# Performance work log

Hardware: AMD Instinct MI355X
Metric: run time of the kernel (lower is better)

The kernel has to match this reference:

```python
import jax, jax.numpy as jnp
import numpy as np

Q_HEADS, KV_HEADS, DIMS, IN_DIMS = 16, 4, 1024, 1024
HEAD_D = DIMS // Q_HEADS            # 64
GROUPS = Q_HEADS // KV_HEADS        # 4
ROPE_BASE = 10000.0


def nd_rope(x, coords):
    """N-D rotary embedding.
    x: [..., s, d]; coords: broadcastable [..., s, a] (float).
    Head dim d is split into a contiguous chunks of d//a; within each chunk
    consecutive pairs (2i, 2i+1) are rotated by angle coord_axis * base^(-2i/(d//a)).
    """
    a = coords.shape[-1]
    d = x.shape[-1]
    dpa = d // a                                  # dims per coordinate axis (even)
    inv_freq = ROPE_BASE ** (-jnp.arange(dpa // 2, dtype=jnp.float32) * (2.0 / dpa))
    angles = coords[..., :, None] * inv_freq      # [..., s, a, dpa//2]
    angles = angles.reshape(angles.shape[:-2] + (d // 2,))
    cos, sin = jnp.cos(angles), jnp.sin(angles)
    xp = x.reshape(x.shape[:-1] + (d // 2, 2))
    x1, x2 = xp[..., 0], xp[..., 1]
    return jnp.stack([x1 * cos - x2 * sin, x1 * sin + x2 * cos], axis=-1).reshape(x.shape)


def setup_inputs() -> dict:
    key = jax.random.key(0)
    k1, k2, k3, k4, k5, k6, k7, k8 = jax.random.split(key, 8)
    B, SQ, SKV, A = 4, 2048, 2048, 2
    q = jax.random.normal(k1, (B, SQ, IN_DIMS), dtype=jnp.float32)
    kv = jax.random.normal(k2, (B, SKV, IN_DIMS), dtype=jnp.float32)
    q_coords = jax.random.randint(k3, (B, SQ, A), 0, 2048, dtype=jnp.int32)
    kv_coords = jax.random.randint(k4, (B, SKV, A), 0, 2048, dtype=jnp.int32)
    s_in = 1.0 / np.sqrt(IN_DIMS)
    Wq = jax.random.normal(k5, (IN_DIMS, Q_HEADS, HEAD_D), dtype=jnp.float32) * s_in
    Wk = jax.random.normal(k6, (IN_DIMS, KV_HEADS, HEAD_D), dtype=jnp.float32) * s_in
    Wv = jax.random.normal(k7, (IN_DIMS, KV_HEADS, HEAD_D), dtype=jnp.float32) * s_in
    Wo = jax.random.normal(k8, (KV_HEADS * HEAD_D, IN_DIMS), dtype=jnp.float32) * (1.0 / np.sqrt(KV_HEADS * HEAD_D))
    return {"q": q, "q_coords": q_coords, "kv": kv, "kv_coords": kv_coords,
            "Wq": Wq, "Wk": Wk, "Wv": Wv, "Wo": Wo}


def reference(q, q_coords, kv, kv_coords, Wq, Wk, Wv, Wo):
    B, SQ = q.shape[0], q.shape[1]
    qp = jnp.einsum('bsi,ihd->bshd', q, Wq)   # [b, sq, q_heads, hd]
    kp = jnp.einsum('bsi,ihd->bshd', kv, Wk)  # [b, skv, kv_heads, hd]
    vp = jnp.einsum('bsi,ihd->bshd', kv, Wv)
    # '... s (h g) d -> ... g h s d' with h=KV_HEADS outer, g=GROUPS inner
    qp = qp.reshape(B, SQ, KV_HEADS, GROUPS, HEAD_D).transpose(0, 3, 2, 1, 4)  # [b,g,h,sq,hd]
    kp = kp.transpose(0, 2, 1, 3)  # [b,h,skv,hd]
    vp = vp.transpose(0, 2, 1, 3)
    qc = q_coords.astype(jnp.float32)[:, None, None]  # [b,1,1,sq,a] -> broadcast over g,h
    kc = kv_coords.astype(jnp.float32)[:, None]       # [b,1,skv,a] -> broadcast over h
    qr = nd_rope(qp, qc)
    kr = nd_rope(kp, kc)
    # NOTE: einops pattern omits g in output -> group axis is SUMMED (faithful to source)
    scores = jnp.einsum('bghsd,bhad->bhsa', qr, kr) / (HEAD_D ** 0.5)
    attn = jax.nn.softmax(scores, axis=-1)
    out = jnp.einsum('bhsa,bhad->bhsd', attn, vp)
    out = out.transpose(0, 2, 1, 3).reshape(B, SQ, KV_HEADS * HEAD_D)
    return out @ Wo
```

## Files before the change

### kernel.cpp

```cpp
#include <hip/hip_runtime.h>

#define BATCH 4
#define SEQQ  2048
#define SEQKV 2048
#define NH    4
#define HD    64
#define IND   1024
#define QSCL 0.18033688011112042f

typedef __attribute__((ext_vector_type(8))) short short8;
typedef __attribute__((ext_vector_type(4))) short s4v;
typedef __attribute__((ext_vector_type(4))) float floatx4;

#if defined(__HIP_DEVICE_COMPILE__) && __has_builtin(__builtin_amdgcn_exp2f)
  #define EXP2(x) __builtin_amdgcn_exp2f(x)
#else
  #define EXP2(x) exp2f(x)
#endif

#if defined(__HIP_DEVICE_COMPILE__)
  #if __has_builtin(__builtin_amdgcn_mfma_f32_16x16x16bf16_1k)
    #define MFMA16(a, b, c) __builtin_amdgcn_mfma_f32_16x16x16bf16_1k(a, b, c, 0, 0, 0)
  #elif __has_builtin(__builtin_amdgcn_mfma_f32_16x16x16_bf16)
    #define MFMA16(a, b, c) __builtin_amdgcn_mfma_f32_16x16x16_bf16(a, b, c, 0, 0, 0)
  #else
    #error "no 16x16x16 bf16 MFMA builtin on gfx950 device pass"
  #endif
#else
  #define MFMA16(a, b, c) (c)
#endif
#define MFMA32(a, b, c) __builtin_amdgcn_mfma_f32_16x16x32_bf16(a, b, c, 0, 0, 0)

__device__ __forceinline__ short f2b(float f) {
    unsigned u; __builtin_memcpy(&u, &f, 4);
    u = (u + 0x7fffu + ((u >> 16) & 1u)) >> 16;
    return (short)u;
}
__device__ __forceinline__ short8 cvt8(const float* p) {
    float4 a = *(const float4*)p;
    float4 b = *(const float4*)(p + 4);
    short8 r;
    r[0] = f2b(a.x); r[1] = f2b(a.y); r[2] = f2b(a.z); r[3] = f2b(a.w);
    r[4] = f2b(b.x); r[5] = f2b(b.y); r[6] = f2b(b.z); r[7] = f2b(b.w);
    return r;
}

__global__ __launch_bounds__(256) void prep_all(
    const float* __restrict__ Wq, const float* __restrict__ Wk,
    const float* __restrict__ Wv, const float* __restrict__ Wo,
    const float* __restrict__ q, const float* __restrict__ kv,
    short* __restrict__ Wq_t, short* __restrict__ Wkv_t, short* __restrict__ Wo_t,
    short* __restrict__ qb, short* __restrict__ kvb) {
    __shared__ short Ts[64][65];
    int blk = blockIdx.x;
    if (blk < 256) {
        int c4 = threadIdx.x & 63, r4 = threadIdx.x >> 6;
        if (blk < 64) {
            int h = blk & 3, ib = blk >> 2;
#pragma unroll 4
            for (int jj = 0; jj < 16; ++jj) {
                int il = r4 * 16 + jj;
                float s = 0.f;
#pragma unroll
                for (int g = 0; g < 4; ++g)
                    s += Wq[(ib * 64 + il) * 1024 + (h * 4 + g) * 64 + c4];
                Ts[il][c4] = f2b(s);
            }
            __syncthreads();
#pragma unroll 4
            for (int jj = 0; jj < 16; ++jj) {
                int dl = r4 * 16 + jj;
                Wq_t[(h * 64 + dl) * 1024 + ib * 64 + c4] = Ts[c4][dl];
            }
        } else if (blk < 192) {
            int t = blk - 64, ss = t >> 6; t &= 63;
            int ib = t >> 2, nb = t & 3;
            const float* W = ss ? Wv : Wk;
#pragma unroll 4
            for (int jj = 0; jj < 16; ++jj) {
                int il = r4 * 16 + jj;
                Ts[il][c4] = f2b(W[(ib * 64 + il) * 256 + nb * 64 + c4]);
            }
            __syncthreads();
#pragma unroll 4
            for (int jj = 0; jj < 16; ++jj) {
                int dl = r4 * 16 + jj;
                Wkv_t[(ss * 256 + nb * 64 + dl) * 1024 + ib * 64 + c4] = Ts[c4][dl];
            }
        } else {
            int t = blk - 192, kb = t >> 4, nb = t & 15;
#pragma unroll 4
            for (int jj = 0; jj < 16; ++jj) {
                int il = r4 * 16 + jj;
                Ts[il][c4] = f2b(Wo[(kb * 64 + il) * 1024 + nb * 64 + c4]);
            }
            __syncthreads();
#pragma unroll 4
            for (int jj = 0; jj < 16; ++jj) {
                int dl = r4 * 16 + jj;
                Wo_t[(nb * 64 + dl) * 256 + kb * 64 + c4] = Ts[c4][dl];
            }
        }
    } else if (blk < 4352) {
        long e = ((long)(blk - 256) * 256 + threadIdx.x) * 8;
        *(short8*)(qb + e) = cvt8(q + e);
    } else {
        long e = ((long)(blk - 4352) * 256 + threadIdx.x) * 8;
        *(short8*)(kvb + e) = cvt8(kv + e);
    }
}

__device__ __forceinline__ void gemm128_body(
    const short* __restrict__ A, const short* __restrict__ Wt, float* __restrict__ C,
    int m0, int n0, int N, int K, short* As, short* Bs) {
    const int t = threadIdx.x;
    const int w = t >> 6, lane = t & 63, ln = lane & 15, quad = lane >> 4;
    const int wm = w >> 1, wn = w & 1;
    const int srow = lane >> 2, skc = (lane & 3) * 8;
    floatx4 acc[4][4];
#pragma unroll
    for (int mt = 0; mt < 4; ++mt)
#pragma unroll
        for (int nt = 0; nt < 4; ++nt) acc[mt][nt] = floatx4{0.f, 0.f, 0.f, 0.f};

    for (int ks = 0; ks < K; ks += 32) {
        __syncthreads();
#pragma unroll
        for (int i = 0; i < 2; ++i) {
            __builtin_amdgcn_global_load_lds(
                (const void*)(A + (long)(m0 + w * 32 + i * 16 + srow) * K + ks + skc),
                (void*)(As + (w * 2 + i) * 512), 16, 0, 0);
            __builtin_amdgcn_global_load_lds(
                (const void*)(Wt + (long)(n0 + w * 32 + i * 16 + srow) * K + ks + skc),
                (void*)(Bs + (w * 2 + i) * 512), 16, 0, 0);
        }
        __syncthreads();
        short8 af[4], bf[4];
#pragma unroll
        for (int mt = 0; mt < 4; ++mt)
            af[mt] = *(const short8*)(As + (wm * 64 + mt * 16 + ln) * 32 + quad * 8);
#pragma unroll
        for (int nt = 0; nt < 4; ++nt)
            bf[nt] = *(const short8*)(Bs + (wn * 64 + nt * 16 + ln) * 32 + quad * 8);
#pragma unroll
        for (int mt = 0; mt < 4; ++mt)
#pragma unroll
            for (int nt = 0; nt < 4; ++nt)
                acc[mt][nt] = MFMA32(af[mt], bf[nt], acc[mt][nt]);
    }
#pragma unroll
    for (int mt = 0; mt < 4; ++mt) {
        int row0 = m0 + wm * 64 + mt * 16 + quad * 4;
#pragma unroll
        for (int nt = 0; nt < 4; ++nt) {
            int col = n0 + wn * 64 + nt * 16 + ln;
#pragma unroll
            for (int r = 0; r < 4; ++r)
                C[(long)(row0 + r) * N + col] = acc[mt][nt][r];
        }
    }
}

__global__ __launch_bounds__(256) void proj_gemm(
    const short* __restrict__ qb, const short* __restrict__ kvb,
    const short* __restrict__ Wq_t, const short* __restrict__ Wkv_t,
    float* __restrict__ Qp, float* __restrict__ KVp) {
    __shared__ __align__(16) short As[128 * 32];
    __shared__ __align__(16) short Bs[128 * 32];
    int id = blockIdx.x;
    if (id < 128)
        gemm128_body(qb, Wq_t, Qp, (id >> 1) * 128, (id & 1) * 128, 256, 1024, As, Bs);
    else {
        int t = id - 128;
        gemm128_body(kvb, Wkv_t, KVp, (t >> 2) * 128, (t & 3) * 128, 512, 1024, As, Bs);
    }
}

__global__ __launch_bounds__(256) void final_gemm(
    const short* __restrict__ Ob, const short* __restrict__ Wo_t, float* __restrict__ out) {
    __shared__ __align__(16) short As[128 * 32];
    __shared__ __align__(16) short Bs[128 * 32];
    gemm128_body(Ob, Wo_t, out, blockIdx.x * 128, blockIdx.y * 128, 1024, 256, As, Bs);
}

__global__ __launch_bounds__(256) void rope_all(
    const float* __restrict__ Qp, const int* __restrict__ qc,
    const float* __restrict__ KVp, const int* __restrict__ kvc,
    short* __restrict__ Qr, short* __restrict__ Kr, short* __restrict__ Vt) {
    __shared__ __align__(16) short Ts[64][72];
    int blk = blockIdx.x;
    if (blk < 8192) {
        bool isq = blk < 4096;
        int idx = (isq ? blk : blk - 4096) * 256 + threadIdx.x;
        int j = idx & 31, h = (idx >> 5) & 3, s = (idx >> 7) & 2047, b = idx >> 18;
        int bs = b * 2048 + s;
        const float* src = isq ? (Qp + (long)bs * 256) : (KVp + (long)bs * 512);
        float2 x = *(const float2*)(src + h * 64 + 2 * j);
        float c = (float)(isq ? qc : kvc)[bs * 2 + (j >> 4)];
        float ang = c * __expf((float)(j & 15) * -0.5756462732485114f);
        float sn, cs; __sincosf(ang, &sn, &cs);
        if (isq) { sn *= QSCL; cs *= QSCL; }
        short2 o; o.x = f2b(x.x * cs - x.y * sn); o.y = f2b(x.x * sn + x.y * cs);
        short* dst = isq ? Qr : Kr;
        *(short2*)(dst + (long)((b * 4 + h) * 2048 + s) * 64 + 2 * j) = o;
    } else {
        int t2 = blk - 8192;
        int bh = t2 & 15, kt = (t2 >> 4) << 6;
        int b = bh >> 2, h = bh & 3;
        {
            int r = threadIdx.x >> 2, c = (threadIdx.x & 3) << 4;
            const float* src = KVp + (long)(b * 2048 + kt + r) * 512 + 256 + h * 64 + c;
#pragma unroll
            for (int j = 0; j < 16; ++j) Ts[c + j][r] = f2b(src[j]);
        }
        __syncthreads();
        {
            int d = threadIdx.x >> 2, c = (threadIdx.x & 3) << 4;
            long dst = ((long)bh * 64 + d) * 2048 + kt + c;
            *(short8*)(Vt + dst)     = *(const short8*)(&Ts[d][c]);
            *(short8*)(Vt + dst + 8) = *(const short8*)(&Ts[d][c + 8]);
        }
    }
}

__global__ __launch_bounds__(256, 4) void attn_kernel(
    const short* __restrict__ Qr, const short* __restrict__ Kr,
    const short* __restrict__ Vt, float* __restrict__ Op, float* __restrict__ Lp) {
    __shared__ __align__(16) short Kls[64 * 64];
    __shared__ __align__(16) short Vls[64 * 64];
    const int blk = blockIdx.x;
    const int bh = blk & 15, sp = (blk >> 4) & 3, qg = blk >> 6;
    const int w = threadIdx.x >> 6, lane = threadIdx.x & 63;
    const int ln = lane & 15, quad = lane >> 4;
    const int q0 = qg * 128 + w * 32;
    const short* Qb = Qr + (long)bh * SEQKV * HD;
    const short* Kb = Kr + (long)bh * SEQKV * HD;
    const short* Vb = Vt + (long)bh * HD * SEQKV;

    const int srow = lane >> 3;
    const int schk = (lane & 7) ^ (srow & 7);
    const long kstage0 = (long)(w * 16 + srow) * HD + schk * 8;
    const long vstage0 = (long)(w * 16 + srow) * SEQKV + schk * 8;

    short8 qf[2][2];
#pragma unroll
    for (int qs = 0; qs < 2; ++qs)
#pragma unroll
        for (int ck = 0; ck < 2; ++ck)
            qf[qs][ck] = *(const short8*)(Qb + (long)(q0 + qs * 16 + ln) * HD + ck * 32 + quad * 8);

    s4v ones;
#pragma unroll
    for (int j = 0; j < 4; ++j) ones[j] = (short)0x3F80;

    floatx4 o[2][4], ol[2];
#pragma unroll
    for (int qs = 0; qs < 2; ++qs) {
        ol[qs] = floatx4{0.f, 0.f, 0.f, 0.f};
#pragma unroll
        for (int nt = 0; nt < 4; ++nt) o[qs][nt] = floatx4{0.f, 0.f, 0.f, 0.f};
    }

    const int ln7 = ln & 7;
    int koff[2];
#pragma unroll
    for (int ck = 0; ck < 2; ++ck) koff[ck] = ln * 64 + ((ck * 4 + quad) ^ ln7) * 8;
    int voff[4];
#pragma unroll
    for (int t = 0; t < 4; ++t) voff[t] = ln * 64 + ((t * 2 + (quad >> 1)) ^ ln7) * 8 + (quad & 1) * 4;

    for (int kt = sp * 512; kt < sp * 512 + 512; kt += 64) {
        __syncthreads();
#pragma unroll
        for (int i = 0; i < 2; ++i) {
            __builtin_amdgcn_global_load_lds(
                (const void*)(Kb + (long)kt * HD + kstage0 + (long)i * 8 * HD),
                (void*)(Kls + (w * 16 + i * 8) * 64), 16, 0, 0);
            __builtin_amdgcn_global_load_lds(
                (const void*)(Vb + kt + vstage0 + (long)i * 8 * SEQKV),
                (void*)(Vls + (w * 16 + i * 8) * 64), 16, 0, 0);
        }
        __syncthreads();

#pragma unroll
        for (int t = 0; t < 4; ++t) {
            short8 a0 = *(const short8*)(Kls + t * 1024 + koff[0]);
            short8 a1 = *(const short8*)(Kls + t * 1024 + koff[1]);
            floatx4 st0 = {0.f, 0.f, 0.f, 0.f}, st1 = {0.f, 0.f, 0.f, 0.f};
            st0 = MFMA32(a0, qf[0][0], st0);
            st1 = MFMA32(a0, qf[1][0], st1);
            st0 = MFMA32(a1, qf[0][1], st0);
            st1 = MFMA32(a1, qf[1][1], st1);
            s4v pt0, pt1;
#pragma unroll
            for (int j = 0; j < 4; ++j) {
                float p0 = EXP2(st0[j]);
                float p1 = EXP2(st1[j]);
                unsigned u0, u1;
                __builtin_memcpy(&u0, &p0, 4); __builtin_memcpy(&u1, &p1, 4);
                pt0[j] = (short)((u0 + 0x8000u) >> 16);
                pt1[j] = (short)((u1 + 0x8000u) >> 16);
            }
#pragma unroll
            for (int nt = 0; nt < 4; ++nt) {
                s4v vf = *(const s4v*)(Vls + nt * 1024 + voff[t]);
                o[0][nt] = MFMA16(vf, pt0, o[0][nt]);
                o[1][nt] = MFMA16(vf, pt1, o[1][nt]);
            }
            ol[0] = MFMA16(ones, pt0, ol[0]);
            ol[1] = MFMA16(ones, pt1, ol[1]);
        }
    }
#pragma unroll
    for (int qs = 0; qs < 2; ++qs) {
        long qrow = (long)(sp * 16 + bh) * 2048 + q0 + qs * 16 + ln;
        if (quad == 0) Lp[qrow] = ol[qs][0];
#pragma unroll
        for (int nt = 0; nt < 4; ++nt)
            *(floatx4*)(Op + qrow * 64 + nt * 16 + quad * 4) = o[qs][nt];
    }
}

__global__ __launch_bounds__(256) void combine_kernel(
    const float* __restrict__ Op, const float* __restrict__ Lp, short* __restrict__ Ob) {
    int row = blockIdx.x * 4 + (threadIdx.x >> 6);
    int d = threadIdx.x & 63;
    int bh = row >> 11, qq = row & 2047;
    int b = bh >> 2, h = bh & 3;
    float os = 0.f, ls = 0.f;
#pragma unroll
    for (int s = 0; s < 4; ++s) {
        long rr = (long)(s * 16 + bh) * 2048 + qq;
        os += Op[rr * 64 + d];
        ls += Lp[rr];
    }
    Ob[((long)(b * 2048 + qq)) * 256 + h * 64 + d] = f2b(os / ls);
}

extern "C" void kernel_launch(void* const* d_in, const int* in_sizes, int n_in,
                              void* d_out, int out_size, void* d_ws, size_t ws_size,
                              hipStream_t stream) {
    const float* q   = (const float*)d_in[0];
    const int*   qc  = (const int*)d_in[1];
    const float* kv  = (const float*)d_in[2];
    const int*   kvc = (const int*)d_in[3];
    const float* Wq  = (const float*)d_in[4];
    const float* Wk  = (const float*)d_in[5];
    const float* Wv  = (const float*)d_in[6];
    const float* Wo  = (const float*)d_in[7];
    float* out = (float*)d_out;

    char* ws = (char*)d_ws;
    const size_t MB = 1024 * 1024;
    short* Wq_t  = (short*)(ws);
    short* Wkv_t = (short*)(ws + MB / 2);
    short* Wo_t  = (short*)(ws + 3 * MB / 2);
    short* qb    = (short*)(ws + 2 * MB);
    short* kvb   = (short*)(ws + 18 * MB);
    float* Qp    = (float*)(ws + 34 * MB);
    float* KVp   = (float*)(ws + 42 * MB);
    short* Qr    = (short*)(ws + 2 * MB);
    short* Kr    = (short*)(ws + 6 * MB);
    short* Vt    = (short*)(ws + 10 * MB);
    short* Ob    = (short*)(ws + 14 * MB);
    float* Opart = (float*)(ws + 18 * MB);
    float* Lpart = (float*)(ws + 50 * MB);

    hipLaunchKernelGGL(prep_all, dim3(8448), dim3(256), 0, stream,
                       Wq, Wk, Wv, Wo, q, kv, Wq_t, Wkv_t, Wo_t, qb, kvb);
    hipLaunchKernelGGL(proj_gemm, dim3(384), dim3(256), 0, stream,
                       qb, kvb, Wq_t, Wkv_t, Qp, KVp);
    hipLaunchKernelGGL(rope_all, dim3(8704), dim3(256), 0, stream,
                       Qp, qc, KVp, kvc, Qr, Kr, Vt);
    hipLaunchKernelGGL(attn_kernel, dim3(1024), dim3(256), 0, stream,
                       Qr, Kr, Vt, Opart, Lpart);
    hipLaunchKernelGGL(combine_kernel, dim3(8192), dim3(256), 0, stream,
                       Opart, Lpart, Ob);
    hipLaunchKernelGGL(final_gemm, dim3(64, 8), dim3(256), 0, stream, Ob, Wo_t, out);
}
```

Baseline: 204.2 us.

## Fuse RoPE and V transpose into projection GEMM epilogue

Removes the separate rope_all kernel by applying the rotary embedding and the bf16 conversion in the projection GEMM epilogue. Adjacent-pair values are exchanged with lane shuffles, and V is written transposed straight from the accumulators. This drops the fp32 Qp/KVp round trip through global memory and one kernel launch. In exchange the epilogue does extra sincos work per row and issues scattered 2-byte stores, and the workspace layout is moved so buffers no longer alias.

```diff
diff --git a/kernel.cpp b/kernel.cpp
--- a/kernel.cpp
+++ b/kernel.cpp
@@ -110,9 +110,12 @@
     }
 }
 
-__device__ __forceinline__ void gemm128_body(
-    const short* __restrict__ A, const short* __restrict__ Wt, float* __restrict__ C,
-    int m0, int n0, int N, int K, short* As, short* Bs) {
+template <int MODE>
+__device__ __forceinline__ void gemm128(
+    const short* __restrict__ A, const short* __restrict__ Wt,
+    int m0, int n0, int N, int K, short* As, short* Bs,
+    float* __restrict__ C, const int* __restrict__ coords,
+    short* __restrict__ ropeDst, short* __restrict__ vDst) {
     const int t = threadIdx.x;
     const int w = t >> 6, lane = t & 63, ln = lane & 15, quad = lane >> 4;
     const int wm = w >> 1, wn = w & 1;
@@ -148,15 +151,65 @@
             for (int nt = 0; nt < 4; ++nt)
                 acc[mt][nt] = MFMA32(af[mt], bf[nt], acc[mt][nt]);
     }
-#pragma unroll
-    for (int mt = 0; mt < 4; ++mt) {
-        int row0 = m0 + wm * 64 + mt * 16 + quad * 4;
-#pragma unroll
-        for (int nt = 0; nt < 4; ++nt) {
-            int col = n0 + wn * 64 + nt * 16 + ln;
-#pragma unroll
-            for (int r = 0; r < 4; ++r)
-                C[(long)(row0 + r) * N + col] = acc[mt][nt][r];
+
+    if (MODE == 0) {
+#pragma unroll
+        for (int mt = 0; mt < 4; ++mt) {
+            int row0 = m0 + wm * 64 + mt * 16 + quad * 4;
+#pragma unroll
+            for (int nt = 0; nt < 4; ++nt) {
+                int col = n0 + wn * 64 + nt * 16 + ln;
+#pragma unroll
+                for (int r = 0; r < 4; ++r)
+                    C[(long)(row0 + r) * N + col] = acc[mt][nt][r];
+            }
+        }
+    } else {
+        const int wn_col = n0 + wn * 64;
+        if (MODE == 1 || wn_col < 256) {
+            const int h = (wn_col >> 6) & 3;
+            const float scl = (MODE == 1) ? QSCL : 1.0f;
+            const float L = -0.5756462732485114f;
+            const float fA = __expf((float)(ln >> 1) * L);
+            const float fB = __expf((float)(8 + (ln >> 1)) * L);
+            const float sgn = (ln & 1) ? 1.0f : -1.0f;
+#pragma unroll
+            for (int mt = 0; mt < 4; ++mt) {
+                int row0 = m0 + wm * 64 + mt * 16 + quad * 4;
+#pragma unroll
+                for (int r = 0; r < 4; ++r) {
+                    int row = row0 + r;
+                    float c0 = (float)coords[row * 2];
+                    float c1 = (float)coords[row * 2 + 1];
+                    float snv[4], csv[4];
+                    __sincosf(c0 * fA, &snv[0], &csv[0]);
+                    __sincosf(c0 * fB, &snv[1], &csv[1]);
+                    __sincosf(c1 * fA, &snv[2], &csv[2]);
+                    __sincosf(c1 * fB, &snv[3], &csv[3]);
+                    long rbase = ((long)((row >> 11) * 4 + h) * 2048 + (row & 2047)) * 64;
+#pragma unroll
+                    for (int nt = 0; nt < 4; ++nt) {
+                        float v = acc[mt][nt][r];
+                        float p = __shfl_xor(v, 1, 64);
+                        float o = v * (csv[nt] * scl) + p * (snv[nt] * (scl * sgn));
+                        ropeDst[rbase + nt * 16 + ln] = f2b(o);
+                    }
+                }
+            }
+        } else {
+            const int h = ((wn_col - 256) >> 6) & 3;
+#pragma unroll
+            for (int mt = 0; mt < 4; ++mt) {
+                int row0 = m0 + wm * 64 + mt * 16 + quad * 4;
+                int b = row0 >> 11, s0 = row0 & 2047;
+#pragma unroll
+                for (int nt = 0; nt < 4; ++nt) {
+                    s4v ov;
+#pragma unroll
+                    for (int r = 0; r < 4; ++r) ov[r] = f2b(acc[mt][nt][r]);
+                    *(s4v*)(vDst + (long)((b * 4 + h) * 64 + nt * 16 + ln) * 2048 + s0) = ov;
+                }
+            }
         }
     }
 }
@@ -164,15 +217,18 @@
 __global__ __launch_bounds__(256) void proj_gemm(
     const short* __restrict__ qb, const short* __restrict__ kvb,
     const short* __restrict__ Wq_t, const short* __restrict__ Wkv_t,
-    float* __restrict__ Qp, float* __restrict__ KVp) {
+    const int* __restrict__ qc, const int* __restrict__ kvc,
+    short* __restrict__ Qr, short* __restrict__ Kr, short* __restrict__ Vt) {
     __shared__ __align__(16) short As[128 * 32];
     __shared__ __align__(16) short Bs[128 * 32];
     int id = blockIdx.x;
     if (id < 128)
-        gemm128_body(qb, Wq_t, Qp, (id >> 1) * 128, (id & 1) * 128, 256, 1024, As, Bs);
+        gemm128<1>(qb, Wq_t, (id >> 1) * 128, (id & 1) * 128, 256, 1024, As, Bs,
+                   nullptr, qc, Qr, nullptr);
     else {
         int t = id - 128;
-        gemm128_body(kvb, Wkv_t, KVp, (t >> 2) * 128, (t & 3) * 128, 512, 1024, As, Bs);
+        gemm128<2>(kvb, Wkv_t, (t >> 2) * 128, (t & 3) * 128, 512, 1024, As, Bs,
+                   nullptr, kvc, Kr, Vt);
     }
 }
 
@@ -180,47 +236,8 @@
     const short* __restrict__ Ob, const short* __restrict__ Wo_t, float* __restrict__ out) {
     __shared__ __align__(16) short As[128 * 32];
     __shared__ __align__(16) short Bs[128 * 32];
-    gemm128_body(Ob, Wo_t, out, blockIdx.x * 128, blockIdx.y * 128, 1024, 256, As, Bs);
-}
-
-__global__ __launch_bounds__(256) void rope_all(
-    const float* __restrict__ Qp, const int* __restrict__ qc,
-    const float* __restrict__ KVp, const int* __restrict__ kvc,
-    short* __restrict__ Qr, short* __restrict__ Kr, short* __restrict__ Vt) {
-    __shared__ __align__(16) short Ts[64][72];
-    int blk = blockIdx.x;
-    if (blk < 8192) {
-        bool isq = blk < 4096;
-        int idx = (isq ? blk : blk - 4096) * 256 + threadIdx.x;
-        int j = idx & 31, h = (idx >> 5) & 3, s = (idx >> 7) & 2047, b = idx >> 18;
-        int bs = b * 2048 + s;
-        const float* src = isq ? (Qp + (long)bs * 256) : (KVp + (long)bs * 512);
-        float2 x = *(const float2*)(src + h * 64 + 2 * j);
-        float c = (float)(isq ? qc : kvc)[bs * 2 + (j >> 4)];
-        float ang = c * __expf((float)(j & 15) * -0.5756462732485114f);
-        float sn, cs; __sincosf(ang, &sn, &cs);
-        if (isq) { sn *= QSCL; cs *= QSCL; }
-        short2 o; o.x = f2b(x.x * cs - x.y * sn); o.y = f2b(x.x * sn + x.y * cs);
-        short* dst = isq ? Qr : Kr;
-        *(short2*)(dst + (long)((b * 4 + h) * 2048 + s) * 64 + 2 * j) = o;
-    } else {
-        int t2 = blk - 8192;
-        int bh = t2 & 15, kt = (t2 >> 4) << 6;
-        int b = bh >> 2, h = bh & 3;
-        {
-            int r = threadIdx.x >> 2, c = (threadIdx.x & 3) << 4;
-            const float* src = KVp + (long)(b * 2048 + kt + r) * 512 + 256 + h * 64 + c;
-#pragma unroll
-            for (int j = 0; j < 16; ++j) Ts[c + j][r] = f2b(src[j]);
-        }
-        __syncthreads();
-        {
-            int d = threadIdx.x >> 2, c = (threadIdx.x & 3) << 4;
-            long dst = ((long)bh * 64 + d) * 2048 + kt + c;
-            *(short8*)(Vt + dst)     = *(const short8*)(&Ts[d][c]);
-            *(short8*)(Vt + dst + 8) = *(const short8*)(&Ts[d][c + 8]);
-        }
-    }
+    gemm128<0>(Ob, Wo_t, blockIdx.x * 128, blockIdx.y * 128, 1024, 256, As, Bs,
+               out, nullptr, nullptr, nullptr);
 }
 
 __global__ __launch_bounds__(256, 4) void attn_kernel(
@@ -357,21 +374,17 @@
     short* Wo_t  = (short*)(ws + 3 * MB / 2);
     short* qb    = (short*)(ws + 2 * MB);
     short* kvb   = (short*)(ws + 18 * MB);
-    float* Qp    = (float*)(ws + 34 * MB);
-    float* KVp   = (float*)(ws + 42 * MB);
-    short* Qr    = (short*)(ws + 2 * MB);
-    short* Kr    = (short*)(ws + 6 * MB);
-    short* Vt    = (short*)(ws + 10 * MB);
-    short* Ob    = (short*)(ws + 14 * MB);
-    float* Opart = (float*)(ws + 18 * MB);
-    float* Lpart = (float*)(ws + 50 * MB);
+    short* Qr    = (short*)(ws + 34 * MB);
+    short* Kr    = (short*)(ws + 38 * MB);
+    short* Vt    = (short*)(ws + 42 * MB);
+    short* Ob    = (short*)(ws + 46 * MB);
+    float* Opart = (float*)(ws + 50 * MB);
+    float* Lpart = (float*)(ws + 82 * MB);
 
     hipLaunchKernelGGL(prep_all, dim3(8448), dim3(256), 0, stream,
                        Wq, Wk, Wv, Wo, q, kv, Wq_t, Wkv_t, Wo_t, qb, kvb);
     hipLaunchKernelGGL(proj_gemm, dim3(384), dim3(256), 0, stream,
-                       qb, kvb, Wq_t, Wkv_t, Qp, KVp);
-    hipLaunchKernelGGL(rope_all, dim3(8704), dim3(256), 0, stream,
-                       Qp, qc, KVp, kvc, Qr, Kr, Vt);
+                       qb, kvb, Wq_t, Wkv_t, qc, kvc, Qr, Kr, Vt);
     hipLaunchKernelGGL(attn_kernel, dim3(1024), dim3(256), 0, stream,
                        Qr, Kr, Vt, Opart, Lpart);
     hipLaunchKernelGGL(combine_kernel, dim3(8192), dim3(256), 0, stream,
```

Result: faster. 193.1 us (-5.4%).
